# Kernel optimization log

Hardware: AMD Instinct MI355X
Metric: run time of the kernel (lower is better)

## Reference

```python
import jax, jax.numpy as jnp
import numpy as np

V = 25
C = 3
EPS = 1e-5
# ntu_pairs (v1, v2): bone[v1-1] = x[v1-1] - x[v2-1]; each v1 appears exactly once
_PAIRS = ((1, 2), (2, 21), (3, 21), (4, 3), (5, 21), (6, 5), (7, 6), (8, 7), (9, 21),
          (10, 9), (11, 10), (12, 11), (13, 1), (14, 13), (15, 14), (16, 15), (17, 1),
          (18, 17), (19, 18), (20, 19), (22, 23), (21, 21), (23, 8), (24, 25), (25, 12))
_parent = np.zeros(V, dtype=np.int32)
for v1, v2 in _PAIRS:
    _parent[v1 - 1] = v2 - 1
PARENT = jnp.asarray(_parent)


def _embed(z, g, b, wa, ba, wb, bb):
    # z: (N, C, V, T); BatchNorm1d over flattened C*V channels (training-mode batch stats)
    N, c, v, T = z.shape
    zf = z.reshape(N, c * v, T)
    mean = zf.mean(axis=(0, 2), keepdims=True)
    var = zf.var(axis=(0, 2), keepdims=True)
    zn = (zf - mean) * jax.lax.rsqrt(var + EPS) * g[None, :, None] + b[None, :, None]
    zn = zn.reshape(N, c, v, T)
    h = jax.nn.relu(jnp.einsum('ncvt,oc->novt', zn, wa) + ba[None, :, None, None])
    return jax.nn.relu(jnp.einsum('nhvt,oh->novt', h, wb) + bb[None, :, None, None])


def reference(x, bn_g1, bn_b1, w1a, b1a, w1b, b1b, bn_g2, bn_b2, w2a, b2a, w2b, b2b):
    N, T, VC = x.shape
    xi = x.reshape(N, T, V, C).transpose(0, 3, 2, 1)  # (N, C, V, T)
    # fused gather-subtract replacing the 25-pair python loop
    bone = xi - xi[:, :, PARENT, :]
    # t_bone[..., :-1] = bone[..., 1:] - bone[..., :-1]; last frame zero
    t_bone = jnp.pad(bone[..., 1:] - bone[..., :-1], ((0, 0), (0, 0), (0, 0), (0, 1)))
    out = _embed(bone, bn_g1, bn_b1, w1a, b1a, w1b, b1b) + \
          _embed(t_bone, bn_g2, bn_b2, w2a, b2a, w2b, b2b)
    return out


def setup_inputs() -> dict:
    key = jax.random.key(0)
    ks = jax.random.split(key, 8)
    N, T = 256, 300
    return {
        'x': jax.random.normal(ks[0], (N, T, V * C), dtype=jnp.float32),
        'bn_g1': jnp.ones((V * C,), jnp.float32),
        'bn_b1': jnp.zeros((V * C,), jnp.float32),
        'w1a': jax.random.normal(ks[1], (64, C), jnp.float32) * 0.3,
        'b1a': jax.random.normal(ks[2], (64,), jnp.float32) * 0.1,
        'w1b': jax.random.normal(ks[3], (64, 64), jnp.float32) * 0.1,
        'b1b': jax.random.normal(ks[4], (64,), jnp.float32) * 0.1,
        'bn_g2': jnp.ones((V * C,), jnp.float32),
        'bn_b2': jnp.zeros((V * C,), jnp.float32),
        'w2a': jax.random.normal(ks[5], (64, C), jnp.float32) * 0.3,
        'b2a': jax.random.normal(ks[6], (64,), jnp.float32) * 0.1,
        'w2b': jax.random.normal(ks[7], (64, 64), jnp.float32) * 0.1,
        'b2b': jax.random.normal(jax.random.fold_in(key, 7), (64,), jnp.float32) * 0.1,
    }
```

## Files before the change

kernel.cpp:

```cpp
#include <hip/hip_runtime.h>
#include <stdint.h>


#define T_ 300

typedef __attribute__((ext_vector_type(8))) short bf16x8;
typedef __attribute__((ext_vector_type(4))) float f32x4;

__device__ __constant__ int PARENT_D[25] = {1,20,20,2,20,4,5,6,20,8,9,10,0,12,13,14,0,16,17,18,20,22,7,24,11};

static __device__ __forceinline__ unsigned short f2bf(float f) {
  unsigned int u = __float_as_uint(f);
  unsigned int r = (u + 0x7FFFu + ((u >> 16) & 1u)) >> 16;
  return (unsigned short)r;
}

__global__ void k0_zero(float* p, int cnt) {
  int i = blockIdx.x * blockDim.x + threadIdx.x;
  if (i < cnt) p[i] = 0.f;
}

__global__ void k1_stats(const float* __restrict__ x, float* __restrict__ stats) {
  __shared__ float rows[76 * 75];
  const int n = blockIdx.x;
  const int s = blockIdx.y;
  const int tid = threadIdx.x;
  const int r0 = s * 75;
  const int nrows = (s < 3) ? 76 : 75;
  const float* xb = x + (size_t)n * (T_ * 75) + (size_t)r0 * 75;
  for (int i = tid; i < nrows * 75; i += 256) rows[i] = xb[i];
  __syncthreads();
  if (tid < 75) {
    const int vv = tid / 3, cc = tid % 3;
    const int pj = PARENT_D[vv] * 3 + cc;
    const int j = tid;
    const int chn = cc * 25 + vv;
    float s0 = 0.f, s1 = 0.f, s2 = 0.f, s3 = 0.f;
    float b = rows[j] - rows[pj];
    for (int r = 0; r < 75; ++r) {
      s0 += b; s1 += b * b;
      if (r0 + r < 299) {
        float bn = rows[(r + 1) * 75 + j] - rows[(r + 1) * 75 + pj];
        float tb = bn - b;
        s2 += tb; s3 += tb * tb;
        b = bn;
      }
    }
    float* sb = stats + (size_t)s * 304;
    atomicAdd(&sb[chn * 2 + 0], s0);
    atomicAdd(&sb[chn * 2 + 1], s1);
    atomicAdd(&sb[150 + chn * 2 + 0], s2);
    atomicAdd(&sb[150 + chn * 2 + 1], s3);
  }
}

__global__ void k2_prep(const float* __restrict__ stats,
                        const float* __restrict__ g1, const float* __restrict__ bb1,
                        const float* __restrict__ w1a, const float* __restrict__ b1a,
                        const float* __restrict__ g2, const float* __restrict__ bb2,
                        const float* __restrict__ w2a, const float* __restrict__ b2a,
                        const float* __restrict__ w1b, const float* __restrict__ w2b,
                        unsigned short* __restrict__ wfA, unsigned short* __restrict__ wB) {
  __shared__ float sc[150], sh[150];
  const int tid = threadIdx.x;
  if (tid < 150) {
    int p = tid / 75, c75 = tid % 75;
    float s = 0.f, sq = 0.f;
    for (int k = 0; k < 4; ++k) {
      s  += stats[k * 304 + p * 150 + c75 * 2 + 0];
      sq += stats[k * 304 + p * 150 + c75 * 2 + 1];
    }
    const float inv = 1.f / 76800.f;
    float mean = s * inv;
    float var = sq * inv - mean * mean;
    var = var < 0.f ? 0.f : var;
    float g  = (p ? g2 : g1)[c75];
    float bb = (p ? bb2 : bb1)[c75];
    float scale = g * rsqrtf(var + 1e-5f);
    sc[tid] = scale;
    sh[tid] = bb - mean * scale;
  }
  __syncthreads();
  for (int idx = tid; idx < 3200; idx += 256) {
    int p = idx / 1600, rm = idx % 1600, v = rm / 64, o = rm % 64;
    const float* wa = p ? w2a : w1a;
    const float* ba = p ? b2a : b1a;
    int base = p * 75;
    float sc0 = sc[base + v], sc1 = sc[base + 25 + v], sc2 = sc[base + 50 + v];
    float sh0 = sh[base + v], sh1 = sh[base + 25 + v], sh2 = sh[base + 50 + v];
    float a0 = wa[o * 3 + 0], a1 = wa[o * 3 + 1], a2 = wa[o * 3 + 2];
    float bias = ba[o] + a0 * sh0 + a1 * sh1 + a2 * sh2;
    unsigned short* d = wfA + (size_t)idx * 8;
    d[0] = f2bf(a0 * sc0); d[1] = f2bf(a1 * sc1); d[2] = f2bf(a2 * sc2);
    d[3] = f2bf(bias);
    d[4] = 0; d[5] = 0; d[6] = 0; d[7] = 0;
  }
  for (int idx = tid; idx < 8192; idx += 256)
    wB[idx] = f2bf(idx < 4096 ? w1b[idx] : w2b[idx - 4096]);
}

__launch_bounds__(320)
__global__ void k3_main(const float* __restrict__ x,
                        const unsigned short* __restrict__ wfA,
                        const unsigned short* __restrict__ wB,
                        const float* __restrict__ b1b,
                        const float* __restrict__ b2b,
                        float* __restrict__ out) {
  __shared__ float Sx[33 * 75];
  __shared__ alignas(16) unsigned short Hs[5][32][72];
  const int tid = threadIdx.x;
  const int wave = tid >> 6;
  const int lane = tid & 63;
  const int q   = lane >> 4;
  const int l15 = lane & 15;
  const int p31 = lane & 31;

  const int bid = blockIdx.x;
  const int chunk = bid % 10;
  const int rem = bid / 10;
  const int vg = rem % 5;
  const int n = rem / 5;
  const int v = vg * 5 + wave;
  const int pv = PARENT_D[v];
  const int tbase = chunk * 32;
  const int nrows = (chunk < 9) ? 33 : 12;

  {
    const float* xb = x + (size_t)n * (T_ * 75) + (size_t)tbase * 75;
    const int total = nrows * 75;
    const int f4 = total >> 2;
    for (int i = tid; i < f4; i += 320)
      ((float4*)Sx)[i] = ((const float4*)xb)[i];
    if (tid < (total & 3)) Sx[(f4 << 2) + tid] = xb[(f4 << 2) + tid];
  }
  __syncthreads();

  float b0 = 0.f, b1 = 0.f, b2 = 0.f, d0 = 0.f, d1 = 0.f, d2 = 0.f;
  if (lane < 32) {
    int t = tbase + p31;
    int tr0 = (t < 299 ? t : 299) - tbase;
    int tr1 = (t + 1 < 299 ? t + 1 : 299) - tbase;
    const float* r0 = Sx + tr0 * 75;
    const float* r1 = Sx + tr1 * 75;
    float xv0 = r0[v*3+0], xv1 = r0[v*3+1], xv2 = r0[v*3+2];
    float xp0 = r0[pv*3+0], xp1 = r0[pv*3+1], xp2 = r0[pv*3+2];
    float yv0 = r1[v*3+0], yv1 = r1[v*3+1], yv2 = r1[v*3+2];
    float yp0 = r1[pv*3+0], yp1 = r1[pv*3+1], yp2 = r1[pv*3+2];
    b0 = xv0 - xp0; b1 = xv1 - xp1; b2 = xv2 - xp2;
    d0 = (yv0 - yp0) - b0; d1 = (yv1 - yp1) - b1; d2 = (yv2 - yp2) - b2;
  }
  float b0s = __shfl(b0, 16 + l15), b1s = __shfl(b1, 16 + l15), b2s = __shfl(b2, 16 + l15);
  float d0s = __shfl(d0, 16 + l15), d1s = __shfl(d1, 16 + l15), d2s = __shfl(d2, 16 + l15);

  bf16x8 zf[2][2];
  {
    bf16x8 z8 = {0,0,0,0,0,0,0,0};
    zf[0][0] = z8; zf[0][1] = z8; zf[1][0] = z8; zf[1][1] = z8;
    if (q == 0) {
      zf[0][0][0]=(short)f2bf(b0);  zf[0][0][1]=(short)f2bf(b1);  zf[0][0][2]=(short)f2bf(b2);  zf[0][0][3]=(short)0x3F80;
      zf[0][1][0]=(short)f2bf(b0s); zf[0][1][1]=(short)f2bf(b1s); zf[0][1][2]=(short)f2bf(b2s); zf[0][1][3]=(short)0x3F80;
      zf[1][0][0]=(short)f2bf(d0);  zf[1][0][1]=(short)f2bf(d1);  zf[1][0][2]=(short)f2bf(d2);  zf[1][0][3]=(short)0x3F80;
      zf[1][1][0]=(short)f2bf(d0s); zf[1][1][1]=(short)f2bf(d1s); zf[1][1][2]=(short)f2bf(d2s); zf[1][1][3]=(short)0x3F80;
    }
  }

  bf16x8 wf[2][4];
#pragma unroll
  for (int p = 0; p < 2; ++p)
#pragma unroll
    for (int to = 0; to < 4; ++to) {
      bf16x8 w = {0,0,0,0,0,0,0,0};
      if (q == 0)
        w = *(const bf16x8*)(wfA + (size_t)((p * 25 + v) * 64 + l15 + 16 * to) * 8);
      wf[p][to] = w;
    }

  f32x4 acc[2][4][2];
  unsigned short (*Hrow)[72] = Hs[wave];

#pragma unroll
  for (int p = 0; p < 2; ++p) {
    f32x4 D[4][2];
#pragma unroll
    for (int to = 0; to < 4; ++to)
#pragma unroll
      for (int tc = 0; tc < 2; ++tc) {
        f32x4 z4 = {0.f, 0.f, 0.f, 0.f};
        D[to][tc] = __builtin_amdgcn_mfma_f32_16x16x32_bf16(wf[p][to], zf[p][tc], z4, 0, 0, 0);
      }
#pragma unroll
    for (int to = 0; to < 4; ++to)
#pragma unroll
      for (int tc = 0; tc < 2; ++tc) {
        f32x4 dd = D[to][tc];
        uint2 pk;
        pk.x = (unsigned)f2bf(fmaxf(dd[0], 0.f)) | ((unsigned)f2bf(fmaxf(dd[1], 0.f)) << 16);
        pk.y = (unsigned)f2bf(fmaxf(dd[2], 0.f)) | ((unsigned)f2bf(fmaxf(dd[3], 0.f)) << 16);
        *(uint2*)&Hrow[l15 + 16 * tc][16 * to + 4 * q] = pk;
      }
    asm volatile("s_waitcnt lgkmcnt(0)" ::: "memory");

    const unsigned short* wbp = wB + (size_t)p * 4096;
    const float* bias = p ? b2b : b1b;
#pragma unroll
    for (int to = 0; to < 4; ++to) {
      f32x4 bq = *(const f32x4*)(bias + 16 * to + 4 * q);
      acc[p][to][0] = bq;
      acc[p][to][1] = bq;
    }
#pragma unroll
    for (int ks = 0; ks < 2; ++ks) {
      bf16x8 wa2[4];
#pragma unroll
      for (int to = 0; to < 4; ++to)
        wa2[to] = *(const bf16x8*)(wbp + (l15 + 16 * to) * 64 + q * 8 + 32 * ks);
#pragma unroll
      for (int tc = 0; tc < 2; ++tc) {
        bf16x8 hb = *(const bf16x8*)&Hrow[l15 + 16 * tc][q * 8 + 32 * ks];
#pragma unroll
        for (int to = 0; to < 4; ++to)
          acc[p][to][tc] = __builtin_amdgcn_mfma_f32_16x16x32_bf16(wa2[to], hb, acc[p][to][tc], 0, 0, 0);
      }
    }
    asm volatile("s_waitcnt lgkmcnt(0)" ::: "memory");
  }

#pragma unroll
  for (int tc = 0; tc < 2; ++tc) {
    int tpos = tbase + 16 * tc + l15;
    if (tpos < 300) {
#pragma unroll
      for (int to = 0; to < 4; ++to)
#pragma unroll
        for (int r = 0; r < 4; ++r) {
          int o = 16 * to + 4 * q + r;
          float val = fmaxf(acc[0][to][tc][r], 0.f) + fmaxf(acc[1][to][tc][r], 0.f);
          out[(((size_t)n * 64 + o) * 25 + v) * 300 + tpos] = val;
        }
    }
  }
}

extern "C" void kernel_launch(void* const* d_in, const int* in_sizes, int n_in,
                              void* d_out, int out_size, void* d_ws, size_t ws_size,
                              hipStream_t stream) {
  const float* x   = (const float*)d_in[0];
  const float* g1  = (const float*)d_in[1];
  const float* bb1 = (const float*)d_in[2];
  const float* w1a = (const float*)d_in[3];
  const float* b1a = (const float*)d_in[4];
  const float* w1b = (const float*)d_in[5];
  const float* b1b = (const float*)d_in[6];
  const float* g2  = (const float*)d_in[7];
  const float* bb2 = (const float*)d_in[8];
  const float* w2a = (const float*)d_in[9];
  const float* b2a = (const float*)d_in[10];
  const float* w2b = (const float*)d_in[11];
  const float* b2b = (const float*)d_in[12];

  float* stats = (float*)d_ws;
  unsigned short* wfA = (unsigned short*)((char*)d_ws + 4864);
  unsigned short* wB  = (unsigned short*)((char*)d_ws + 4864 + 51200);

  hipLaunchKernelGGL(k0_zero, dim3(5), dim3(256), 0, stream, stats, 1216);
  hipLaunchKernelGGL(k1_stats, dim3(256, 4), dim3(256), 0, stream, x, stats);
  hipLaunchKernelGGL(k2_prep, dim3(1), dim3(256), 0, stream, stats,
                     g1, bb1, w1a, b1a, g2, bb2, w2a, b2a, w1b, w2b, wfA, wB);
  hipLaunchKernelGGL(k3_main, dim3(12800), dim3(320), 0, stream, x, wfA, wB, b1b, b2b, (float*)d_out);
}
```

Baseline: 756.3 us.

## Drop shared-memory x staging, load joints per wave directly from global

The main kernel no longer stages a 33-row slab of x in LDS with a block-wide barrier. Each wave now reads its own joint and parent coordinates straight from global memory, with the upper half-wave loading frame t+1, and gets the temporal difference through a shuffle. Blocks shrink to four independent waves with launch bounds (256,2) and a remapped grid, which removes the barrier and most of the LDS use. In exchange, each wave issues scattered, uncoalesced global reads, and the same x rows are read again by every joint's wave, relying on cache hits.

Measured after the change: 718.5 us. -5.0%, faster.

```diff
diff --git a/kernel.cpp b/kernel.cpp
--- a/kernel.cpp
+++ b/kernel.cpp
@@ -99,15 +99,14 @@
     wB[idx] = f2bf(idx < 4096 ? w1b[idx] : w2b[idx - 4096]);
 }
 
-__launch_bounds__(320)
+__launch_bounds__(256, 2)
 __global__ void k3_main(const float* __restrict__ x,
                         const unsigned short* __restrict__ wfA,
                         const unsigned short* __restrict__ wB,
                         const float* __restrict__ b1b,
                         const float* __restrict__ b2b,
                         float* __restrict__ out) {
-  __shared__ float Sx[33 * 75];
-  __shared__ alignas(16) unsigned short Hs[5][32][72];
+  __shared__ alignas(16) unsigned short Hs[4][32][72];
   const int tid = threadIdx.x;
   const int wave = tid >> 6;
   const int lane = tid & 63;
@@ -115,39 +114,24 @@
   const int l15 = lane & 15;
   const int p31 = lane & 31;
 
-  const int bid = blockIdx.x;
-  const int chunk = bid % 10;
-  const int rem = bid / 10;
-  const int vg = rem % 5;
-  const int n = rem / 5;
-  const int v = vg * 5 + wave;
+  const int wid = blockIdx.x * 4 + wave;
+  const int chunk = wid % 10;
+  const int rem = wid / 10;
+  const int v = rem % 25;
+  const int n = rem / 25;
   const int pv = PARENT_D[v];
   const int tbase = chunk * 32;
-  const int nrows = (chunk < 9) ? 33 : 12;
-
+
+  float b0, b1, b2, d0, d1, d2;
   {
-    const float* xb = x + (size_t)n * (T_ * 75) + (size_t)tbase * 75;
-    const int total = nrows * 75;
-    const int f4 = total >> 2;
-    for (int i = tid; i < f4; i += 320)
-      ((float4*)Sx)[i] = ((const float4*)xb)[i];
-    if (tid < (total & 3)) Sx[(f4 << 2) + tid] = xb[(f4 << 2) + tid];
-  }
-  __syncthreads();
-
-  float b0 = 0.f, b1 = 0.f, b2 = 0.f, d0 = 0.f, d1 = 0.f, d2 = 0.f;
-  if (lane < 32) {
-    int t = tbase + p31;
-    int tr0 = (t < 299 ? t : 299) - tbase;
-    int tr1 = (t + 1 < 299 ? t + 1 : 299) - tbase;
-    const float* r0 = Sx + tr0 * 75;
-    const float* r1 = Sx + tr1 * 75;
-    float xv0 = r0[v*3+0], xv1 = r0[v*3+1], xv2 = r0[v*3+2];
-    float xp0 = r0[pv*3+0], xp1 = r0[pv*3+1], xp2 = r0[pv*3+2];
-    float yv0 = r1[v*3+0], yv1 = r1[v*3+1], yv2 = r1[v*3+2];
-    float yp0 = r1[pv*3+0], yp1 = r1[pv*3+1], yp2 = r1[pv*3+2];
-    b0 = xv0 - xp0; b1 = xv1 - xp1; b2 = xv2 - xp2;
-    d0 = (yv0 - yp0) - b0; d1 = (yv1 - yp1) - b1; d2 = (yv2 - yp2) - b2;
+    int t = tbase + p31 + (lane >> 5);
+    int tr = t < 299 ? t : 299;
+    const float* r = x + (size_t)n * (T_ * 75) + (size_t)tr * 75;
+    float u0 = r[v*3+0],  u1 = r[v*3+1],  u2 = r[v*3+2];
+    float w0 = r[pv*3+0], w1 = r[pv*3+1], w2 = r[pv*3+2];
+    b0 = u0 - w0; b1 = u1 - w1; b2 = u2 - w2;
+    float n0 = __shfl(b0, p31 + 32), n1 = __shfl(b1, p31 + 32), n2 = __shfl(b2, p31 + 32);
+    d0 = n0 - b0; d1 = n1 - b1; d2 = n2 - b2;
   }
   float b0s = __shfl(b0, 16 + l15), b1s = __shfl(b1, 16 + l15), b2s = __shfl(b2, 16 + l15);
   float d0s = __shfl(d0, 16 + l15), d1s = __shfl(d1, 16 + l15), d2s = __shfl(d2, 16 + l15);
@@ -266,5 +250,5 @@
   hipLaunchKernelGGL(k1_stats, dim3(256, 4), dim3(256), 0, stream, x, stats);
   hipLaunchKernelGGL(k2_prep, dim3(1), dim3(256), 0, stream, stats,
                      g1, bb1, w1a, b1a, g2, bb2, w2a, b2a, w1b, w2b, wfA, wB);
-  hipLaunchKernelGGL(k3_main, dim3(12800), dim3(320), 0, stream, x, wfA, wB, b1b, b2b, (float*)d_out);
-}
+  hipLaunchKernelGGL(k3_main, dim3(16000), dim3(256), 0, stream, x, wfA, wB, b1b, b2b, (float*)d_out);
+}
```
